# Performance work log

Measured on AMD Instinct MI355X. Metric: run time of the kernel, lower is better.

Reference implementation:

```python
import jax, jax.numpy as jnp
import numpy as np

BETA = 0.9
THR = 1.0
ALPHA = 2.0  # snntorch ATan surrogate default

@jax.custom_vjp
def spike(x):
    # Heaviside spike with ATan surrogate gradient (snntorch default)
    return (x > 0).astype(x.dtype)

def _spike_fwd(x):
    return spike(x), x

def _spike_bwd(x, g):
    grad = (ALPHA / 2.0) / (1.0 + (jnp.pi / 2.0 * ALPHA * x) ** 2)
    return (g * grad,)

spike.defvjp(_spike_fwd, _spike_bwd)

def setup_inputs() -> dict:
    key = jax.random.key(0)
    k1, k2, k3 = jax.random.split(key, 3)
    T, B, NI, NH, NO = 250, 256, 700, 1024, 20
    input_spikes = (jax.random.uniform(k1, (T, B, NI)) < 0.1).astype(jnp.float32)
    W1 = jax.random.normal(k2, (NH, NI), dtype=jnp.float32) / np.float32(np.sqrt(NI))
    W2 = jax.random.normal(k3, (NO, NH), dtype=jnp.float32) / np.float32(np.sqrt(NH))
    return {"input_spikes": input_spikes, "W1": W1, "W2": W2}

def reference(input_spikes, W1, W2):
    # fc1 over all timesteps in one GEMM: [T,B,NI] x [NH,NI] -> [T,B,NH]
    cur1 = jnp.einsum('tbi,hi->tbh', input_spikes, W1)

    # snntorch Leaky (reset_mechanism='subtract'):
    #   reset = detach(heaviside(mem_prev - thr))
    #   mem   = beta*mem_prev + cur - reset*thr
    #   spk   = heaviside(mem - thr)
    def lif_step(mem, c):
        reset = jax.lax.stop_gradient(spike(mem - THR))
        mem = BETA * mem + c - reset * THR
        spk = spike(mem - THR)
        return mem, spk

    mem0 = jnp.zeros(cur1.shape[1:], cur1.dtype)
    _, spk1 = jax.lax.scan(lif_step, mem0, cur1)  # [T,B,NH]

    # fc2 over all timesteps: [T,B,NH] x [NO,NH] -> [T,B,NO]
    cur2 = jnp.einsum('tbh,oh->tbo', spk1, W2)

    # Readout: Leaky with reset_mechanism='none' -> mem = beta*mem + cur
    def ro_step(mem, c):
        mem = BETA * mem + c
        return mem, mem

    m0 = jnp.zeros(cur2.shape[1:], cur2.dtype)
    _, mem_out_rec = jax.lax.scan(ro_step, m0, cur2)  # [T,B,NO]

    out_rec = jax.nn.softmax(mem_out_rec, axis=2)  # torch softmax dim=1 on [B,NO]
    return mem_out_rec, out_rec
```

## Files before the change

### kernel.cpp

```cpp
#include <hip/hip_runtime.h>
#include <hip/hip_bf16.h>
#include <cstdint>

#define T_STEPS 250
#define BATCH   256
#define NI      700
#define NH      1024
#define NO      20
#define BETAF   0.9f
#define KPAD    704
#define KT_N    22
#define KCAT    2112

typedef __attribute__((ext_vector_type(8))) short bf16x8;
typedef __attribute__((ext_vector_type(4))) float f32x4;

static __device__ __forceinline__ unsigned short f2bu(float x) {
    union { __hip_bfloat16 h; unsigned short u; } c;
    c.h = __float2bfloat16(x);
    return c.u;
}
static __device__ __forceinline__ float b2f(unsigned short u) {
    union { __hip_bfloat16 h; unsigned short u; } c;
    c.u = u;
    return __bfloat162float(c.h);
}

__global__ __launch_bounds__(256) void k0_init(const float* __restrict__ W1,
                                               const float* __restrict__ W2,
                                               float* __restrict__ W2T,
                                               float* __restrict__ mem1,
                                               unsigned short* __restrict__ Bcat) {
    int idx = blockIdx.x * 256 + threadIdx.x;
    if (idx < BATCH * NH) mem1[idx] = 0.f;
    if (idx < NH * NO) {
        int h = idx / NO, o = idx % NO;
        W2T[idx] = W2[o * NH + h];
    }
    if (idx < NH * KPAD) {
        int n = idx / KPAD, k = idx % KPAD;
        float w = (k < NI) ? W1[n * NI + k] : 0.f;
        unsigned short hu = f2bu(w);
        float r1 = w - b2f(hu);
        unsigned short mu = f2bu(r1);
        float r2 = r1 - b2f(mu);
        unsigned short lu = f2bu(r2);
        unsigned short* row = Bcat + (size_t)n * KCAT + k;
        row[0]        = hu;
        row[KPAD]     = mu;
        row[2 * KPAD] = lu;
    }
}

__global__ __launch_bounds__(256) void k1_cvt(const float* __restrict__ A,
                                              unsigned short* __restrict__ Abf,
                                              int rows) {
    int idx = blockIdx.x * 256 + threadIdx.x;
    int r = idx / 176, q = idx - r * 176;
    if (r >= rows) return;
    int k = q * 4;
    ushort4 o = make_ushort4(0, 0, 0, 0);
    if (k < NI) {
        float4 v = *(const float4*)(A + (size_t)r * NI + k);
        o.x = f2bu(v.x); o.y = f2bu(v.y); o.z = f2bu(v.z); o.w = f2bu(v.w);
    }
    *(ushort4*)(Abf + (size_t)r * KPAD + k) = o;
}

__global__ __launch_bounds__(256) void k2_fc1(const unsigned short* __restrict__ Abf,
                                              const unsigned short* __restrict__ Bcat,
                                              float* __restrict__ C) {
    __shared__ unsigned short As[2][128 * 32];
    __shared__ unsigned short Bs[2][3][128 * 32];
    const int tid  = threadIdx.x;
    const int lane = tid & 63;
    const int wv   = tid >> 6;

    int nwg = gridDim.x, bid = blockIdx.x, w;
    if ((nwg & 7) == 0) w = (bid & 7) * (nwg >> 3) + (bid >> 3);
    else                w = bid;
    const int brow = (w >> 3) * 128;
    const int bn   = (w & 7) * 128;
    const int wm   = (wv >> 1) * 64;
    const int wn   = (wv & 1) * 64;

    f32x4 acc[4][4];
#pragma unroll
    for (int i = 0; i < 4; ++i)
#pragma unroll
        for (int j = 0; j < 4; ++j) acc[i][j] = (f32x4){0.f, 0.f, 0.f, 0.f};

    auto stage = [&](const unsigned short* gbase, int rstride, int kcol,
                     unsigned short* lds) {
#pragma unroll
        for (int j = 0; j < 2; ++j) {
            int c   = wv * 128 + j * 64 + lane;
            int row = c >> 2;
            int lk  = ((c & 3) ^ ((row >> 1) & 3)) * 8;
            const unsigned short* src = gbase + (size_t)row * rstride + kcol + lk;
            __builtin_amdgcn_global_load_lds(
                (const __attribute__((address_space(1))) void*)src,
                (__attribute__((address_space(3))) void*)(lds + (wv * 128 + j * 64) * 8),
                16, 0, 0);
        }
    };

    const unsigned short* Ab = Abf + (size_t)brow * KPAD;
    const unsigned short* Bb = Bcat + (size_t)bn * KCAT;

    const int frow = lane & 15;
    const int fsl  = (((lane >> 4) & 3) ^ ((frow >> 1) & 3)) * 8;

    stage(Ab, KPAD, 0, As[0]);
#pragma unroll
    for (int s = 0; s < 3; ++s) stage(Bb, KCAT, s * KPAD, Bs[0][s]);
    __syncthreads();

    for (int kt = 0; kt < KT_N; ++kt) {
        const int cur = kt & 1;
        if (kt + 1 < KT_N) {
            stage(Ab, KPAD, (kt + 1) * 32, As[cur ^ 1]);
#pragma unroll
            for (int s = 0; s < 3; ++s)
                stage(Bb, KCAT, s * KPAD + (kt + 1) * 32, Bs[cur ^ 1][s]);
        }

        const unsigned short* Ac = As[cur];
        bf16x8 a[4];
#pragma unroll
        for (int i = 0; i < 4; ++i)
            a[i] = *(const bf16x8*)&Ac[(wm + i * 16 + frow) * 32 + fsl];
#pragma unroll
        for (int s = 0; s < 3; ++s) {
#pragma unroll
            for (int j = 0; j < 4; ++j) {
                bf16x8 b = *(const bf16x8*)&Bs[cur][s][(wn + j * 16 + frow) * 32 + fsl];
#pragma unroll
                for (int i = 0; i < 4; ++i)
                    acc[i][j] = __builtin_amdgcn_mfma_f32_16x16x32_bf16(a[i], b, acc[i][j], 0, 0, 0);
            }
        }
        __syncthreads();
    }

#pragma unroll
    for (int i = 0; i < 4; ++i) {
#pragma unroll
        for (int j = 0; j < 4; ++j) {
            int col  = bn + wn + j * 16 + (lane & 15);
            int row0 = brow + wm + i * 16 + ((lane >> 4) << 2);
#pragma unroll
            for (int q = 0; q < 4; ++q)
                C[(size_t)(row0 + q) * NH + col] = acc[i][j][q];
        }
    }
}

__global__ __launch_bounds__(256) void k3_lif(const float* __restrict__ cur1,
                                              float* __restrict__ mem1,
                                              unsigned long long* __restrict__ bits,
                                              int TC) {
    int b = blockIdx.x >> 2;
    int hg = blockIdx.x & 3;
    int h = hg * 256 + threadIdx.x;
    const size_t S = (size_t)BATCH * NH;
    const float* p = cur1 + (size_t)b * NH + h;
    unsigned long long* bp = bits + (size_t)b * 16 + hg * 4 + (threadIdx.x >> 6);
    const bool lead = (threadIdx.x & 63) == 0;
    float mem = mem1[b * NH + h];

#define LIF_STEP(cv, t)                                                        \
    {                                                                          \
        float reset = (mem > 1.0f) ? 1.0f : 0.0f;                              \
        mem = fmaf(BETAF, mem, (cv)) - reset;                                  \
        unsigned long long mk = __ballot(mem > 1.0f);                          \
        if (lead) bp[(size_t)(t) * (BATCH * 16)] = mk;                         \
    }

    float c0 = (0 < TC) ? p[0] : 0.f;
    float c1 = (1 < TC) ? p[S] : 0.f;
    float c2 = (2 < TC) ? p[2 * S] : 0.f;
    float c3 = (3 < TC) ? p[3 * S] : 0.f;
    int tc = 0;
    for (; tc + 4 <= TC; tc += 4) {
        LIF_STEP(c0, tc + 0); if (tc + 4 < TC) c0 = p[(size_t)(tc + 4) * S];
        LIF_STEP(c1, tc + 1); if (tc + 5 < TC) c1 = p[(size_t)(tc + 5) * S];
        LIF_STEP(c2, tc + 2); if (tc + 6 < TC) c2 = p[(size_t)(tc + 6) * S];
        LIF_STEP(c3, tc + 3); if (tc + 7 < TC) c3 = p[(size_t)(tc + 7) * S];
    }
    for (; tc < TC; ++tc) { float c = p[(size_t)tc * S]; LIF_STEP(c, tc); }
#undef LIF_STEP
    mem1[b * NH + h] = mem;
}

__global__ __launch_bounds__(256) void k4_fc2(const unsigned long long* __restrict__ bits,
                                              const float* __restrict__ W2T,
                                              float* __restrict__ cur2) {
    int row = blockIdx.x * 4 + (threadIdx.x >> 6);
    int lane = threadIdx.x & 63;
    bool act = lane < NO;
    unsigned long long mv = (lane < 16) ? bits[(size_t)row * 16 + lane] : 0ULL;
    const float* W = W2T + (act ? lane : 0);
    float p0 = 0.f, p1 = 0.f, p2 = 0.f, p3 = 0.f;
#pragma unroll 1
    for (int wseg = 0; wseg < 16; ++wseg) {
        unsigned long long m = __shfl(mv, wseg);
        int base = wseg * 64;
        while (m) {
            int  b0 = __ffsll(m) - 1;            m &= m - 1;
            bool v1 = m != 0;
            int  b1 = v1 ? __ffsll(m) - 1 : 0;   m &= m - 1;
            bool v2 = m != 0;
            int  b2 = v2 ? __ffsll(m) - 1 : 0;   m &= m - 1;
            bool v3 = m != 0;
            int  b3 = v3 ? __ffsll(m) - 1 : 0;   m &= m - 1;
            float w0 = W[(base + b0) * NO];
            float w1 = W[(base + b1) * NO];
            float w2 = W[(base + b2) * NO];
            float w3 = W[(base + b3) * NO];
            p0 += w0;
            p1 += v1 ? w1 : 0.f;
            p2 += v2 ? w2 : 0.f;
            p3 += v3 ? w3 : 0.f;
        }
    }
    if (act) cur2[(size_t)row * NO + lane] = (p0 + p1) + (p2 + p3);
}

__global__ __launch_bounds__(256) void k5_readout(const float* __restrict__ cur2,
                                                  float* __restrict__ out_mem,
                                                  float* __restrict__ out_sm) {
    int b = blockIdx.x * 8 + (threadIdx.x >> 5);
    int o = threadIdx.x & 31;
    bool act = o < NO;
    const float* p = cur2 + (size_t)b * NO + (act ? o : 0);
    float mem = 0.f;
    float nxt = p[0];
    for (int t = 0; t < T_STEPS; ++t) {
        float c = nxt;
        if (t + 1 < T_STEPS) nxt = p[(size_t)(t + 1) * BATCH * NO];
        mem = fmaf(BETAF, mem, c);
        float e = act ? __expf(mem) : 0.f;
        float s = e;
#pragma unroll
        for (int off = 16; off; off >>= 1) s += __shfl_xor(s, off, 32);
        if (act) {
            int base = (t * BATCH + b) * NO;
            out_mem[base + o] = mem;
            out_sm[base + o] = __fdividef(e, s);
        }
    }
}

extern "C" void kernel_launch(void* const* d_in, const int* in_sizes, int n_in,
                              void* d_out, int out_size, void* d_ws, size_t ws_size,
                              hipStream_t stream) {
    const float* spikes = (const float*)d_in[0];
    const float* W1     = (const float*)d_in[1];
    const float* W2     = (const float*)d_in[2];
    float* out_mem = (float*)d_out;
    float* out_sm  = out_mem + (size_t)T_STEPS * BATCH * NO;

    char* ws = (char*)d_ws;
    size_t off = 0;
    auto alloc = [&](size_t bytes) -> char* {
        off = (off + 255) & ~(size_t)255;
        char* p = ws + off;
        off += bytes;
        return p;
    };
    float*          W2T  = (float*)alloc((size_t)NH * NO * 4);
    float*          mem1 = (float*)alloc((size_t)BATCH * NH * 4);
    float*          cur2 = (float*)alloc((size_t)T_STEPS * BATCH * NO * 4);
    unsigned short* Bcat = (unsigned short*)alloc((size_t)NH * KCAT * 2);

    size_t fixed = (off + 255) & ~(size_t)255;
    size_t rem = ws_size > fixed ? ws_size - fixed : 0;
    size_t per_t = (size_t)BATCH * NH * 4 + (size_t)BATCH * KPAD * 2
                 + (size_t)BATCH * 16 * 8 + 768;
    int TC = (int)(rem / per_t);
    if (TC > T_STEPS) TC = T_STEPS;
    if (TC < 1) TC = 1;
    float*              cur1 = (float*)alloc((size_t)TC * BATCH * NH * 4);
    unsigned short*     Abf  = (unsigned short*)alloc((size_t)TC * BATCH * KPAD * 2);
    unsigned long long* bits = (unsigned long long*)alloc((size_t)TC * BATCH * 16 * 8);

    k0_init<<<(NH * KPAD + 255) / 256, 256, 0, stream>>>(W1, W2, W2T, mem1, Bcat);

    for (int t0 = 0; t0 < T_STEPS; t0 += TC) {
        int tc = T_STEPS - t0 < TC ? T_STEPS - t0 : TC;
        int rows = tc * BATCH;
        k1_cvt<<<(rows * 176 + 255) / 256, 256, 0, stream>>>(
            spikes + (size_t)t0 * BATCH * NI, Abf, rows);
        int nwg = (rows / 128) * 8;
        k2_fc1<<<nwg, 256, 0, stream>>>(Abf, Bcat, cur1);
        k3_lif<<<1024, 256, 0, stream>>>(cur1, mem1, bits, tc);
        k4_fc2<<<tc * 64, 256, 0, stream>>>(bits, W2T, cur2 + (size_t)t0 * BATCH * NO);
    }

    k5_readout<<<32, 256, 0, stream>>>(cur2, out_mem, out_sm);
}
```

Baseline: 602.0 us.

## Flatten fc1 K-loop over concatenated weights and split fc2 rows across waves

The fc1 GEMM now walks the concatenated K dimension as 66 single tiles instead of 22 triple-B tiles. This shrinks LDS use for B to one double-buffered tile. It replaces __syncthreads with explicit vmcnt waits, raw barriers and MFMA priority boosts so that loads overlap with compute, while the A tile index wraps around. The fc2 spike-gather kernel now gives each output row a whole workgroup, with each wave handling a quarter of the hidden bits, and reduces partial sums through shared memory to shorten each wave's serial loop. The risks are more barriers per K-step, a hand-tuned vmcnt that must match the number of issued loads, and four times as many fc2 workgroups.

```diff
diff --git a/kernel.cpp b/kernel.cpp
--- a/kernel.cpp
+++ b/kernel.cpp
@@ -9,8 +9,8 @@
 #define NO      20
 #define BETAF   0.9f
 #define KPAD    704
-#define KT_N    22
 #define KCAT    2112
+#define NKT     66
 
 typedef __attribute__((ext_vector_type(8))) short bf16x8;
 typedef __attribute__((ext_vector_type(4))) float f32x4;
@@ -71,7 +71,7 @@
                                               const unsigned short* __restrict__ Bcat,
                                               float* __restrict__ C) {
     __shared__ unsigned short As[2][128 * 32];
-    __shared__ unsigned short Bs[2][3][128 * 32];
+    __shared__ unsigned short Bs[2][128 * 32];
     const int tid  = threadIdx.x;
     const int lane = tid & 63;
     const int wv   = tid >> 6;
@@ -111,37 +111,45 @@
     const int frow = lane & 15;
     const int fsl  = (((lane >> 4) & 3) ^ ((frow >> 1) & 3)) * 8;
 
-    stage(Ab, KPAD, 0, As[0]);
-#pragma unroll
-    for (int s = 0; s < 3; ++s) stage(Bb, KCAT, s * KPAD, Bs[0][s]);
-    __syncthreads();
-
-    for (int kt = 0; kt < KT_N; ++kt) {
-        const int cur = kt & 1;
-        if (kt + 1 < KT_N) {
-            stage(Ab, KPAD, (kt + 1) * 32, As[cur ^ 1]);
-#pragma unroll
-            for (int s = 0; s < 3; ++s)
-                stage(Bb, KCAT, s * KPAD + (kt + 1) * 32, Bs[cur ^ 1][s]);
-        }
-
+    auto compute = [&](int cur) {
         const unsigned short* Ac = As[cur];
+        const unsigned short* Bc = Bs[cur];
         bf16x8 a[4];
 #pragma unroll
         for (int i = 0; i < 4; ++i)
             a[i] = *(const bf16x8*)&Ac[(wm + i * 16 + frow) * 32 + fsl];
-#pragma unroll
-        for (int s = 0; s < 3; ++s) {
-#pragma unroll
-            for (int j = 0; j < 4; ++j) {
-                bf16x8 b = *(const bf16x8*)&Bs[cur][s][(wn + j * 16 + frow) * 32 + fsl];
-#pragma unroll
-                for (int i = 0; i < 4; ++i)
-                    acc[i][j] = __builtin_amdgcn_mfma_f32_16x16x32_bf16(a[i], b, acc[i][j], 0, 0, 0);
-            }
-        }
-        __syncthreads();
-    }
+        __builtin_amdgcn_s_setprio(1);
+#pragma unroll
+        for (int j = 0; j < 4; ++j) {
+            bf16x8 b = *(const bf16x8*)&Bc[(wn + j * 16 + frow) * 32 + fsl];
+#pragma unroll
+            for (int i = 0; i < 4; ++i)
+                acc[i][j] = __builtin_amdgcn_mfma_f32_16x16x32_bf16(a[i], b, acc[i][j], 0, 0, 0);
+        }
+        __builtin_amdgcn_s_setprio(0);
+    };
+
+    stage(Ab, KPAD, 0, As[0]);
+    stage(Bb, KCAT, 0, Bs[0]);
+
+    int akn = 32;
+    for (int kt = 0; kt < NKT - 1; ++kt) {
+        const int cur = kt & 1;
+        stage(Ab, KPAD, akn, As[cur ^ 1]);
+        stage(Bb, KCAT, (kt + 1) * 32, Bs[cur ^ 1]);
+        akn += 32; if (akn == KPAD) akn = 0;
+
+        asm volatile("s_waitcnt vmcnt(4)" ::: "memory");
+        __builtin_amdgcn_s_barrier();
+        __builtin_amdgcn_sched_barrier(0);
+        compute(cur);
+        __builtin_amdgcn_s_barrier();
+        __builtin_amdgcn_sched_barrier(0);
+    }
+    asm volatile("s_waitcnt vmcnt(0)" ::: "memory");
+    __builtin_amdgcn_s_barrier();
+    __builtin_amdgcn_sched_barrier(0);
+    compute((NKT - 1) & 1);
 
 #pragma unroll
     for (int i = 0; i < 4; ++i) {
@@ -196,35 +204,35 @@
 __global__ __launch_bounds__(256) void k4_fc2(const unsigned long long* __restrict__ bits,
                                               const float* __restrict__ W2T,
                                               float* __restrict__ cur2) {
-    int row = blockIdx.x * 4 + (threadIdx.x >> 6);
+    __shared__ float part[4][NO];
+    int row  = blockIdx.x;
+    int wv   = threadIdx.x >> 6;
     int lane = threadIdx.x & 63;
     bool act = lane < NO;
-    unsigned long long mv = (lane < 16) ? bits[(size_t)row * 16 + lane] : 0ULL;
+    unsigned long long mv = (lane < 4) ? bits[(size_t)row * 16 + wv * 4 + lane] : 0ULL;
     const float* W = W2T + (act ? lane : 0);
-    float p0 = 0.f, p1 = 0.f, p2 = 0.f, p3 = 0.f;
-#pragma unroll 1
-    for (int wseg = 0; wseg < 16; ++wseg) {
-        unsigned long long m = __shfl(mv, wseg);
-        int base = wseg * 64;
+    float p0 = 0.f, p1 = 0.f;
+#pragma unroll
+    for (int i = 0; i < 4; ++i) {
+        unsigned long long m = __shfl(mv, i);
+        int base = (wv * 4 + i) * 64;
         while (m) {
             int  b0 = __ffsll(m) - 1;            m &= m - 1;
             bool v1 = m != 0;
             int  b1 = v1 ? __ffsll(m) - 1 : 0;   m &= m - 1;
-            bool v2 = m != 0;
-            int  b2 = v2 ? __ffsll(m) - 1 : 0;   m &= m - 1;
-            bool v3 = m != 0;
-            int  b3 = v3 ? __ffsll(m) - 1 : 0;   m &= m - 1;
             float w0 = W[(base + b0) * NO];
             float w1 = W[(base + b1) * NO];
-            float w2 = W[(base + b2) * NO];
-            float w3 = W[(base + b3) * NO];
             p0 += w0;
             p1 += v1 ? w1 : 0.f;
-            p2 += v2 ? w2 : 0.f;
-            p3 += v3 ? w3 : 0.f;
-        }
-    }
-    if (act) cur2[(size_t)row * NO + lane] = (p0 + p1) + (p2 + p3);
+        }
+    }
+    float p = p0 + p1;
+    if (wv != 0 && act) part[wv][lane] = p;
+    __syncthreads();
+    if (wv == 0 && act) {
+        p += part[1][lane] + part[2][lane] + part[3][lane];
+        cur2[(size_t)row * NO + lane] = p;
+    }
 }
 
 __global__ __launch_bounds__(256) void k5_readout(const float* __restrict__ cur2,
@@ -295,7 +303,7 @@
         int nwg = (rows / 128) * 8;
         k2_fc1<<<nwg, 256, 0, stream>>>(Abf, Bcat, cur1);
         k3_lif<<<1024, 256, 0, stream>>>(cur1, mem1, bits, tc);
-        k4_fc2<<<tc * 64, 256, 0, stream>>>(bits, W2T, cur2 + (size_t)t0 * BATCH * NO);
+        k4_fc2<<<rows, 256, 0, stream>>>(bits, W2T, cur2 + (size_t)t0 * BATCH * NO);
     }
 
     k5_readout<<<32, 256, 0, stream>>>(cur2, out_mem, out_sm);
```

Result: no change. 603.9 us (+0.3%).
